# Kernel tuning notes

Hardware: AMD Instinct MI355X
Metric: run time of the kernel (lower is better)

## Reference

```python
import jax, jax.numpy as jnp
import numpy as np
import math

IN_C, OUT_C = 64, 128
OUT_C1 = int((OUT_C - IN_C) * 0.3 + IN_C)  # 83
OUT_C2 = int((OUT_C - IN_C) * 0.6 + IN_C)  # 102
OUT_C3 = OUT_C                              # 128
RESIDUE_RATIO = 0.5
R_RES = math.sqrt(RESIDUE_RATIO)
R_SC = math.sqrt(1.0 - RESIDUE_RATIO)
PRELU_INIT = 0.25
POST_MEAN = (1.0 - PRELU_INIT) / math.sqrt(2.0 * math.pi)
_POST_EX2 = (1.0 + PRELU_INIT ** 2) / 2.0
POST_STDV = math.sqrt(_POST_EX2 - POST_MEAN ** 2)


def _conv1x1_weight(key, out_c, in_c):
    # torch Conv1d custom init: normal_, then divide by per-out-channel L2 norm
    w = jax.random.normal(key, (out_c, in_c), dtype=jnp.float32)
    norm = jnp.sqrt(jnp.sum(w ** 2, axis=1, keepdims=True) + 1e-8)
    return w / norm


def cprelu(x, w):
    # x: [B, C, N], w: [C]
    y = jnp.where(x >= 0, x, x * w[None, :, None])
    return (y - POST_MEAN) / POST_STDV


def setup_inputs() -> dict:
    key = jax.random.key(0)
    ks = jax.random.split(key, 8)
    x = jax.random.normal(ks[0], (16, IN_C, 8192), dtype=jnp.float32)
    conn = jax.random.uniform(ks[1], (4096, 8192), dtype=jnp.float32)
    return {
        "x": x,
        "conn": conn,
        "w1": _conv1x1_weight(ks[2], OUT_C1, IN_C),
        "b1": jnp.zeros((OUT_C1,), jnp.float32),
        "p1": jnp.full((OUT_C1,), PRELU_INIT, jnp.float32),
        "w2": _conv1x1_weight(ks[3], OUT_C2, OUT_C1),
        "b2": jnp.zeros((OUT_C2,), jnp.float32),
        "p2": jnp.full((OUT_C2,), PRELU_INIT, jnp.float32),
        "wm": _conv1x1_weight(ks[4], OUT_C3, OUT_C2),
        "bm": jnp.zeros((OUT_C3,), jnp.float32),
        "p3": jnp.full((OUT_C3,), PRELU_INIT, jnp.float32),
        "ws": _conv1x1_weight(ks[5], OUT_C, IN_C),
        "bs": jnp.zeros((OUT_C,), jnp.float32),
    }


def _forward(x, conn, w1, b1, p1, w2, b2, p2, wm, bm, p3, ws, bs):
    # self-connection matrix: binary mask of per-row argmax entries (ties kept)
    sc = (conn - jnp.max(conn, axis=1, keepdims=True) >= 0).astype(jnp.float32)

    # residue branch: 1x1 conv -> CPReLU -> 1x1 conv -> CPReLU -> Meshconv -> CPReLU
    h = cprelu(jnp.einsum('bcn,oc->bon', x, w1) + b1[None, :, None], p1)
    h = cprelu(jnp.einsum('bcn,oc->bon', h, w2) + b2[None, :, None], p2)
    h = jnp.einsum('bcn,oc->bon', h, wm) + bm[None, :, None]      # [B, C3, Nin]
    h = jnp.einsum('oi,bci->bco', conn, h)                         # mesh pooling -> [B, C3, Nout]
    res = cprelu(h, p3)

    # shortcut branch: Meshconv with self_connection_matrix (1x1 conv + pooled gather)
    s = jnp.einsum('bcn,oc->bon', x, ws) + bs[None, :, None]       # [B, OUT_C, Nin]
    s = jnp.einsum('oi,bci->bco', sc, s)                           # [B, OUT_C, Nout]

    return s * R_SC + res * R_RES


def reference(x, conn, w1, b1, p1, w2, b2, p2, wm, bm, p3, ws, bs):
    return _forward(x, conn, w1, b1, p1, w2, b2, p2, wm, bm, p3, ws, bs)
```

## Files before the change

kernel.cpp:

```cpp
#include <hip/hip_runtime.h>
#include <hip/hip_bf16.h>
#include <stdint.h>

using bf16x8 = __attribute__((ext_vector_type(8))) __bf16;
using bf16x4 = __attribute__((ext_vector_type(4))) __bf16;
using f32x4  = __attribute__((ext_vector_type(4))) float;

typedef const uint32_t __attribute__((address_space(1)))* gas_ptr;
typedef uint32_t __attribute__((address_space(3)))* las_ptr;

__device__ __forceinline__ void load_lds16(const void* g, void* l) {
    __builtin_amdgcn_global_load_lds((gas_ptr)g, (las_ptr)l, 16, 0, 0);
}

#define PM  0.29920671030107454f
#define PIS 1.5046096f
#define RHALF 0.70710678118654752f

__global__ __launch_bounds__(256) void k_prep(const float* __restrict__ w1,
                                              const float* __restrict__ w2,
                                              const float* __restrict__ wm,
                                              const float* __restrict__ wsw,
                                              __bf16* __restrict__ W1p,
                                              __bf16* __restrict__ W2p,
                                              __bf16* __restrict__ WMp,
                                              __bf16* __restrict__ WSp)
{
    const int id = blockIdx.x * 256 + threadIdx.x;
    const int stride = gridDim.x * 256;
    for (int i = id; i < 96 * 64; i += stride) {
        int oc = i >> 6, ic = i & 63;
        W1p[i] = (__bf16)((oc < 83) ? w1[oc * 64 + ic] : 0.f);
    }
    for (int i = id; i < 112 * 96; i += stride) {
        int oc = i / 96, ic = i % 96;
        W2p[i] = (__bf16)((oc < 102 && ic < 83) ? w2[oc * 83 + ic] : 0.f);
    }
    for (int i = id; i < 128 * 128; i += stride) {
        int oc = i >> 7, ic = i & 127;
        WMp[i] = (__bf16)((ic < 102) ? wm[oc * 102 + ic] : 0.f);
    }
    for (int i = id; i < 128 * 64; i += stride) {
        WSp[i] = (__bf16)wsw[i];
    }
}

__global__ __launch_bounds__(256) void k_conv(const float* __restrict__ conn,
                                              __bf16* __restrict__ cb,
                                              size_t rowstride,
                                              int* __restrict__ cnt,
                                              int* __restrict__ idx)
{
    const int o = blockIdx.x;
    const int t = threadIdx.x;
    const float* row = conn + (size_t)o * 8192;
    float4 v[8];
    float m = -1e30f;
#pragma unroll
    for (int q = 0; q < 8; q++) {
        v[q] = *(const float4*)(row + (size_t)(q * 256 + t) * 4);
        m = fmaxf(m, fmaxf(fmaxf(v[q].x, v[q].y), fmaxf(v[q].z, v[q].w)));
    }
    __syncthreads();
    __bf16* drow = cb + (size_t)o * rowstride;
#pragma unroll
    for (int q = 0; q < 8; q++) {
        bf16x4 w;
        w[0] = (__bf16)v[q].x; w[1] = (__bf16)v[q].y;
        w[2] = (__bf16)v[q].z; w[3] = (__bf16)v[q].w;
        *(bf16x4*)(drow + (size_t)(q * 256 + t) * 4) = w;
    }
#pragma unroll
    for (int off = 32; off > 0; off >>= 1) m = fmaxf(m, __shfl_down(m, off, 64));
    __shared__ float wmax[4];
    __shared__ int scnt;
    if ((t & 63) == 0) wmax[t >> 6] = m;
    if (t == 0) scnt = 0;
    __syncthreads();
    const float rmax = fmaxf(fmaxf(wmax[0], wmax[1]), fmaxf(wmax[2], wmax[3]));
#pragma unroll
    for (int q = 0; q < 8; q++) {
        float vv[4] = {v[q].x, v[q].y, v[q].z, v[q].w};
#pragma unroll
        for (int e = 0; e < 4; e++) {
            if (vv[e] >= rmax) {
                int p = atomicAdd(&scnt, 1);
                if (p < 16) idx[o * 16 + p] = (q * 256 + t) * 4 + e;
            }
        }
    }
    __syncthreads();
    if (t == 0) cnt[o] = scnt < 16 ? scnt : 16;
}

template<int KS>
__device__ __forceinline__ f32x4 mfma_tile(const __bf16* __restrict__ W, int wstride, int mt,
                                           const __bf16* B, int bstride, int nt, int lane)
{
    f32x4 acc = {0.f, 0.f, 0.f, 0.f};
    const int l15 = lane & 15;
    const int kg  = (lane >> 4) << 3;
    const __bf16* wp = W + (mt * 16 + l15) * wstride + kg;
    const __bf16* bp = B + (nt * 16 + l15) * bstride + kg;
#pragma unroll
    for (int ks = 0; ks < KS; ks++) {
        bf16x8 av = *(const bf16x8*)(wp + ks * 32);
        bf16x8 bv = *(const bf16x8*)(bp + ks * 32);
        acc = __builtin_amdgcn_mfma_f32_16x16x32_bf16(av, bv, acc, 0, 0, 0);
    }
    return acc;
}

__global__ __launch_bounds__(256) void k_chain(
    const float* __restrict__ x,
    const float* __restrict__ b1, const float* __restrict__ p1,
    const float* __restrict__ b2, const float* __restrict__ p2,
    const float* __restrict__ bm, const float* __restrict__ bs,
    const __bf16* __restrict__ W1p, const __bf16* __restrict__ W2p,
    const __bf16* __restrict__ WMp, const __bf16* __restrict__ WSp,
    __bf16* __restrict__ h3, __bf16* __restrict__ s_t)
{
    __shared__ __bf16 buf0[64 * 136];
    __shared__ __bf16 H1t[64 * 104];
    __shared__ float  bl[672];
    float* b1l = bl;       float* p1l = bl + 96;
    float* b2l = bl + 192; float* p2l = bl + 304;
    float* bml = bl + 416; float* bsl = bl + 544;

    const int t = threadIdx.x, lane = t & 63, wid = t >> 6;
    const int b = blockIdx.y;
    const int p0 = blockIdx.x * 64;

    for (int i = t; i < 96; i += 256)  { b1l[i] = (i < 83)  ? b1[i] : 0.f; p1l[i] = (i < 83)  ? p1[i] : 0.f; }
    for (int i = t; i < 112; i += 256) { b2l[i] = (i < 102) ? b2[i] : 0.f; p2l[i] = (i < 102) ? p2[i] : 0.f; }
    for (int i = t; i < 128; i += 256) { bml[i] = bm[i]; bsl[i] = bs[i]; }

    {
        const int p = t & 63;
        const int cg = t >> 6;
#pragma unroll 4
        for (int it = 0; it < 16; it++) {
            int c = it * 4 + cg;
            buf0[p * 72 + c] = (__bf16)x[((size_t)b * 64 + c) * 8192 + p0 + p];
        }
    }
    __syncthreads();

    const int quad4 = (lane >> 4) << 2;
    const int l15 = lane & 15;

    for (int tt = wid; tt < 32; tt += 4) {
        int mt = tt >> 2, nt = tt & 3;
        f32x4 a = mfma_tile<2>(WSp, 64, mt, buf0, 72, nt, lane);
        int ocb = mt * 16 + quad4;
        int pos = nt * 16 + l15;
        bf16x4 ov;
#pragma unroll
        for (int r = 0; r < 4; r++) ov[r] = (__bf16)(a[r] + bsl[ocb + r]);
        *(bf16x4*)(s_t + ((size_t)b * 8192 + p0 + pos) * 128 + ocb) = ov;
    }
    for (int tt = wid; tt < 24; tt += 4) {
        int mt = tt >> 2, nt = tt & 3;
        f32x4 a = mfma_tile<2>(W1p, 64, mt, buf0, 72, nt, lane);
        int ocb = mt * 16 + quad4;
        int pos = nt * 16 + l15;
        bf16x4 ov;
#pragma unroll
        for (int r = 0; r < 4; r++) {
            float v = a[r] + b1l[ocb + r];
            v = (v >= 0.f) ? v : v * p1l[ocb + r];
            ov[r] = (__bf16)((v - PM) * PIS);
        }
        *(bf16x4*)(&H1t[pos * 104 + ocb]) = ov;
    }
    __syncthreads();

    for (int tt = wid; tt < 28; tt += 4) {
        int mt = tt >> 2, nt = tt & 3;
        f32x4 a = mfma_tile<3>(W2p, 96, mt, H1t, 104, nt, lane);
        int ocb = mt * 16 + quad4;
        int pos = nt * 16 + l15;
        bf16x4 ov;
#pragma unroll
        for (int r = 0; r < 4; r++) {
            float v = a[r] + b2l[ocb + r];
            v = (v >= 0.f) ? v : v * p2l[ocb + r];
            ov[r] = (__bf16)((v - PM) * PIS);
        }
        *(bf16x4*)(&buf0[pos * 136 + ocb]) = ov;
    }
    for (int i = t; i < 64 * 16; i += 256) {
        int pos = i >> 4, c = 112 + (i & 15);
        buf0[pos * 136 + c] = (__bf16)0.f;
    }
    __syncthreads();

    for (int tt = wid; tt < 32; tt += 4) {
        int mt = tt >> 2, nt = tt & 3;
        f32x4 a = mfma_tile<4>(WMp, 128, mt, buf0, 136, nt, lane);
        int ocb = mt * 16 + quad4;
        int pos = nt * 16 + l15;
#pragma unroll
        for (int r = 0; r < 4; r++)
            h3[((size_t)b * 128 + ocb + r) * 8192 + p0 + pos] = (__bf16)(a[r] + bml[ocb + r]);
    }
}

__global__ __launch_bounds__(256) void k_gemm(const __bf16* __restrict__ A,
                                              const __bf16* __restrict__ B,
                                              size_t bstride,
                                              float* __restrict__ C0,
                                              float* __restrict__ C1,
                                              int KH)
{
    __shared__ __bf16 la[128 * 32];
    __shared__ __bf16 lb[128 * 32];
    const int t = threadIdx.x;
    const int lane = t & 63;
    const int wid = t >> 6;
    const int tM = blockIdx.y * 128;
    const int tN = blockIdx.x * 128;
    const int kz = blockIdx.z;
    const int k0 = kz * KH;
    float* __restrict__ C = kz ? C1 : C0;
    const int wm2 = (wid & 1) * 64;
    const int wn2 = (wid >> 1) * 64;

    f32x4 acc[4][4];
    const f32x4 zero = {0.f, 0.f, 0.f, 0.f};
#pragma unroll
    for (int i = 0; i < 4; i++)
#pragma unroll
        for (int j = 0; j < 4; j++) acc[i][j] = zero;

    const __bf16* Ab = A + (size_t)tM * 8192;
    const __bf16* Bb = B + (size_t)tN * bstride;
    const int ar = t >> 2;
    const int ak = ((t & 3) ^ ((t >> 3) & 3)) * 8;
    const int l15 = lane & 15;
    const int q = lane >> 4;

    int aoff[4], boff[4];
#pragma unroll
    for (int i = 0; i < 4; i++) {
        int row = wm2 + i * 16 + l15;
        aoff[i] = row * 32 + ((q ^ ((row >> 1) & 3)) * 8);
    }
#pragma unroll
    for (int j = 0; j < 4; j++) {
        int row = wn2 + j * 16 + l15;
        boff[j] = row * 32 + ((q ^ ((row >> 1) & 3)) * 8);
    }

    for (int kt = k0; kt < k0 + KH; kt += 32) {
        load_lds16(Ab + (size_t)ar * 8192 + kt + ak, la + t * 8);
        load_lds16(Ab + (size_t)(64 + ar) * 8192 + kt + ak, la + 2048 + t * 8);
        load_lds16(Bb + (size_t)ar * bstride + kt + ak, lb + t * 8);
        load_lds16(Bb + (size_t)(64 + ar) * bstride + kt + ak, lb + 2048 + t * 8);
        __syncthreads();
        bf16x8 af[4], bfr[4];
#pragma unroll
        for (int i = 0; i < 4; i++) af[i]  = *(const bf16x8*)(la + aoff[i]);
#pragma unroll
        for (int j = 0; j < 4; j++) bfr[j] = *(const bf16x8*)(lb + boff[j]);
#pragma unroll
        for (int i = 0; i < 4; i++)
#pragma unroll
            for (int j = 0; j < 4; j++)
                acc[i][j] = __builtin_amdgcn_mfma_f32_16x16x32_bf16(af[i], bfr[j], acc[i][j], 0, 0, 0);
        __syncthreads();
    }

    const int quad4 = (lane >> 4) * 4;
#pragma unroll
    for (int i = 0; i < 4; i++) {
        int gm = tM + wm2 + i * 16 + quad4;
#pragma unroll
        for (int j = 0; j < 4; j++) {
            int gn = tN + wn2 + j * 16 + l15;
#pragma unroll
            for (int r = 0; r < 4; r++)
                C[(size_t)(gm + r) * 4096 + gn] = acc[i][j][r];
        }
    }
}

__global__ __launch_bounds__(256) void k_combine(float* __restrict__ out,
                                                 const float* __restrict__ P1,
                                                 int nsplit,
                                                 const __bf16* __restrict__ s_t,
                                                 const int* __restrict__ idx,
                                                 const int* __restrict__ cnt,
                                                 const float* __restrict__ p3)
{
    __shared__ float sp[64][133];
    const int b = blockIdx.y;
    const int o0 = blockIdx.x * 64;
    const int t = threadIdx.x;

    {
        const int ol = t >> 2;
        const int part = t & 3;
        const int o = o0 + ol;
        const int n = cnt[o];
        float acc[32];
#pragma unroll
        for (int j = 0; j < 32; j++) acc[j] = 0.f;
        for (int k = 0; k < n; k++) {
            const int i = idx[o * 16 + k];
            const __bf16* row = s_t + ((size_t)b * 8192 + i) * 128 + part * 32;
#pragma unroll
            for (int j = 0; j < 32; j += 8) {
                bf16x8 v = *(const bf16x8*)(row + j);
#pragma unroll
                for (int u = 0; u < 8; u++) acc[j + u] += (float)v[u];
            }
        }
#pragma unroll
        for (int j = 0; j < 32; j++) sp[ol][part * 32 + j] = acc[j];
    }
    __syncthreads();

    if (nsplit == 2) {
        for (int rr = 0; rr < 32; rr++) {
            const int c = rr * 4 + (t >> 6);
            const int o = t & 63;
            const size_t oi = ((size_t)b * 128 + c) * 4096 + o0 + o;
            float v = out[oi] + P1[oi];
            const float pw = p3[c];
            float y = (v >= 0.f) ? v : v * pw;
            y = (y - PM) * PIS;
            out[oi] = sp[o][c] * RHALF + y * RHALF;
        }
    } else {
        for (int rr = 0; rr < 32; rr++) {
            const int c = rr * 4 + (t >> 6);
            const int o = t & 63;
            const size_t oi = ((size_t)b * 128 + c) * 4096 + o0 + o;
            float v = out[oi];
            const float pw = p3[c];
            float y = (v >= 0.f) ? v : v * pw;
            y = (y - PM) * PIS;
            out[oi] = sp[o][c] * RHALF + y * RHALF;
        }
    }
}

extern "C" void kernel_launch(void* const* d_in, const int* in_sizes, int n_in,
                              void* d_out, int out_size, void* d_ws, size_t ws_size,
                              hipStream_t stream) {
    (void)in_sizes; (void)n_in; (void)out_size;
    const float* x    = (const float*)d_in[0];
    const float* conn = (const float*)d_in[1];
    const float* w1   = (const float*)d_in[2];
    const float* b1   = (const float*)d_in[3];
    const float* p1   = (const float*)d_in[4];
    const float* w2   = (const float*)d_in[5];
    const float* b2   = (const float*)d_in[6];
    const float* p2   = (const float*)d_in[7];
    const float* wm   = (const float*)d_in[8];
    const float* bm   = (const float*)d_in[9];
    const float* p3   = (const float*)d_in[10];
    const float* wsw  = (const float*)d_in[11];
    const float* bs   = (const float*)d_in[12];
    float* out = (float*)d_out;

    char* ws = (char*)d_ws;
    __bf16* h3  = (__bf16*)(ws);
    __bf16* s_t = (__bf16*)(ws + 33554432);
    __bf16* W1p = (__bf16*)(ws + 67108864);
    __bf16* W2p = (__bf16*)(ws + 67108864 + 12288);
    __bf16* WMp = (__bf16*)(ws + 67108864 + 33792);
    __bf16* WSp = (__bf16*)(ws + 67108864 + 66560);
    int* idx = (int*)(ws + 67108864 + 82944);
    int* cnt = (int*)(ws + 67108864 + 82944 + 262144);
    const size_t p1_off    = 67108864 + 82944 + 262144 + 16384;
    float* Pk1 = (float*)(ws + p1_off);
    const size_t connb_off = p1_off + 33554432;

    __bf16* connb;
    size_t  cstride;
    if (ws_size >= connb_off + (size_t)4096 * 8192 * 2) {
        connb = (__bf16*)(ws + connb_off);
        cstride = 8192;
    } else {
        connb = (__bf16*)const_cast<float*>(conn);
        cstride = 16384;
    }
    const int nsplit = (ws_size >= p1_off + 33554432) ? 2 : 1;
    const int KH = 8192 / nsplit;

    k_prep<<<32, 256, 0, stream>>>(w1, w2, wm, wsw, W1p, W2p, WMp, WSp);
    k_conv<<<4096, 256, 0, stream>>>(conn, connb, cstride, cnt, idx);
    k_chain<<<dim3(8192 / 64, 16), 256, 0, stream>>>(x, b1, p1, b2, p2, bm, bs,
                                                     W1p, W2p, WMp, WSp, h3, s_t);
    k_gemm<<<dim3(4096 / 128, 2048 / 128, nsplit), 256, 0, stream>>>(h3, connb, cstride,
                                                                     out, Pk1, KH);
    k_combine<<<dim3(4096 / 64, 16), 256, 0, stream>>>(out, Pk1, nsplit, s_t, idx, cnt, p3);
}
```

Baseline: 523.4 us.

## Widen GEMM K-tile to 64 with XOR swizzle and coalesce h3 stores via LDS

The main GEMM now loads a 64-wide K slice per iteration instead of 32. It uses an 8-way XOR swizzle in LDS and precomputed per-row pointers, which halves the barrier count per unit of work and packs more MFMAs between syncs. Launch bounds now request 4 blocks per SM. In the chain kernel, the h3 output is first staged transposed in a shared buffer that reuses the H1t storage, then written with 16-byte coalesced stores instead of scattered 2-byte stores. The trade-off is doubled LDS per GEMM block and a new occupancy hint that may cap registers.

```diff
diff --git a/kernel.cpp b/kernel.cpp
--- a/kernel.cpp
+++ b/kernel.cpp
@@ -121,8 +121,10 @@
     __bf16* __restrict__ h3, __bf16* __restrict__ s_t)
 {
     __shared__ __bf16 buf0[64 * 136];
-    __shared__ __bf16 H1t[64 * 104];
+    __shared__ __bf16 un[128 * 72];
     __shared__ float  bl[672];
+    __bf16* H1t  = un;
+    __bf16* OutT = un;
     float* b1l = bl;       float* p1l = bl + 96;
     float* b2l = bl + 192; float* p2l = bl + 304;
     float* bml = bl + 416; float* bsl = bl + 544;
@@ -202,19 +204,28 @@
         int pos = nt * 16 + l15;
 #pragma unroll
         for (int r = 0; r < 4; r++)
-            h3[((size_t)b * 128 + ocb + r) * 8192 + p0 + pos] = (__bf16)(a[r] + bml[ocb + r]);
-    }
-}
-
-__global__ __launch_bounds__(256) void k_gemm(const __bf16* __restrict__ A,
-                                              const __bf16* __restrict__ B,
-                                              size_t bstride,
-                                              float* __restrict__ C0,
-                                              float* __restrict__ C1,
-                                              int KH)
-{
-    __shared__ __bf16 la[128 * 32];
-    __shared__ __bf16 lb[128 * 32];
+            OutT[(ocb + r) * 72 + pos] = (__bf16)(a[r] + bml[ocb + r]);
+    }
+    __syncthreads();
+
+#pragma unroll
+    for (int it = 0; it < 4; it++) {
+        int lin = it * 256 + t;
+        int ch = lin >> 3, pc = lin & 7;
+        bf16x8 v = *(const bf16x8*)(OutT + ch * 72 + pc * 8);
+        *(bf16x8*)(h3 + ((size_t)b * 128 + ch) * 8192 + p0 + pc * 8) = v;
+    }
+}
+
+__global__ __launch_bounds__(256, 4) void k_gemm(const __bf16* __restrict__ A,
+                                                 const __bf16* __restrict__ B,
+                                                 size_t bstride,
+                                                 float* __restrict__ C0,
+                                                 float* __restrict__ C1,
+                                                 int KH)
+{
+    __shared__ __bf16 la[128 * 64];
+    __shared__ __bf16 lb[128 * 64];
     const int t = threadIdx.x;
     const int lane = t & 63;
     const int wid = t >> 6;
@@ -233,41 +244,52 @@
 #pragma unroll
         for (int j = 0; j < 4; j++) acc[i][j] = zero;
 
-    const __bf16* Ab = A + (size_t)tM * 8192;
-    const __bf16* Bb = B + (size_t)tN * bstride;
-    const int ar = t >> 2;
-    const int ak = ((t & 3) ^ ((t >> 3) & 3)) * 8;
+    const int tr = t >> 3;
+    const int sc = (t & 7) ^ (tr & 7);
+    const __bf16* pA[4];
+    const __bf16* pB[4];
+#pragma unroll
+    for (int i = 0; i < 4; i++) {
+        pA[i] = A + (size_t)(tM + i * 32 + tr) * 8192 + k0 + sc * 8;
+        pB[i] = B + (size_t)(tN + i * 32 + tr) * bstride + k0 + sc * 8;
+    }
+
     const int l15 = lane & 15;
     const int q = lane >> 4;
-
     int aoff[4], boff[4];
 #pragma unroll
     for (int i = 0; i < 4; i++) {
         int row = wm2 + i * 16 + l15;
-        aoff[i] = row * 32 + ((q ^ ((row >> 1) & 3)) * 8);
+        aoff[i] = row * 64 + ((q ^ (row & 7)) * 8);
     }
 #pragma unroll
     for (int j = 0; j < 4; j++) {
         int row = wn2 + j * 16 + l15;
-        boff[j] = row * 32 + ((q ^ ((row >> 1) & 3)) * 8);
-    }
-
-    for (int kt = k0; kt < k0 + KH; kt += 32) {
-        load_lds16(Ab + (size_t)ar * 8192 + kt + ak, la + t * 8);
-        load_lds16(Ab + (size_t)(64 + ar) * 8192 + kt + ak, la + 2048 + t * 8);
-        load_lds16(Bb + (size_t)ar * bstride + kt + ak, lb + t * 8);
-        load_lds16(Bb + (size_t)(64 + ar) * bstride + kt + ak, lb + 2048 + t * 8);
+        boff[j] = row * 64 + ((q ^ (row & 7)) * 8);
+    }
+
+    const int iters = KH >> 6;
+    for (int it = 0; it < iters; it++) {
+#pragma unroll
+        for (int i = 0; i < 4; i++) load_lds16(pA[i], la + (i * 256 + t) * 8);
+#pragma unroll
+        for (int i = 0; i < 4; i++) load_lds16(pB[i], lb + (i * 256 + t) * 8);
+#pragma unroll
+        for (int i = 0; i < 4; i++) { pA[i] += 64; pB[i] += 64; }
         __syncthreads();
-        bf16x8 af[4], bfr[4];
-#pragma unroll
-        for (int i = 0; i < 4; i++) af[i]  = *(const bf16x8*)(la + aoff[i]);
-#pragma unroll
-        for (int j = 0; j < 4; j++) bfr[j] = *(const bf16x8*)(lb + boff[j]);
-#pragma unroll
-        for (int i = 0; i < 4; i++)
-#pragma unroll
-            for (int j = 0; j < 4; j++)
-                acc[i][j] = __builtin_amdgcn_mfma_f32_16x16x32_bf16(af[i], bfr[j], acc[i][j], 0, 0, 0);
+#pragma unroll
+        for (int ks = 0; ks < 2; ks++) {
+            bf16x8 af[4], bfr[4];
+#pragma unroll
+            for (int i = 0; i < 4; i++) af[i]  = *(const bf16x8*)(la + (aoff[i] ^ (ks << 5)));
+#pragma unroll
+            for (int j = 0; j < 4; j++) bfr[j] = *(const bf16x8*)(lb + (boff[j] ^ (ks << 5)));
+#pragma unroll
+            for (int i = 0; i < 4; i++)
+#pragma unroll
+                for (int j = 0; j < 4; j++)
+                    acc[i][j] = __builtin_amdgcn_mfma_f32_16x16x32_bf16(af[i], bfr[j], acc[i][j], 0, 0, 0);
+        }
         __syncthreads();
     }
 
```

New measurement: 485.8 us. 1.08x faster.
